# Optimization experiments

Measured on AMD Instinct MI355X. Metric: run time of the kernel, lower is better.

## Reference

```python
import jax, jax.numpy as jnp
import numpy as np
from jax import lax

SCALE = 128.0        # x/y/w/h scale = model input size
MIN_SCORE = 0.5      # min_score_thresh
IOU_THRESH = 0.3     # mediapipe min_suppression_threshold
MAX_DET = 64         # fixed detection slots (jit-safe replacement for dynamic list)
NUM_ANCHORS = 896


def _decode(raw_boxes, anchors):
    # raw_boxes [B,A,16], anchors [A,4] = (x_center, y_center, w, h)
    ax, ay, aw, ah = anchors[:, 0], anchors[:, 1], anchors[:, 2], anchors[:, 3]
    xc = raw_boxes[..., 0] / SCALE * aw + ax
    yc = raw_boxes[..., 1] / SCALE * ah + ay
    w = raw_boxes[..., 2] / SCALE * aw
    h = raw_boxes[..., 3] / SCALE * ah
    box = jnp.stack([yc - h / 2, xc - w / 2, yc + h / 2, xc + w / 2], axis=-1)  # [B,A,4] ymin,xmin,ymax,xmax
    kp = raw_boxes[..., 4:16].reshape(*raw_boxes.shape[:-1], 6, 2)  # [B,A,6,2] (x,y)
    kpx = kp[..., 0] / SCALE * aw[:, None] + ax[:, None]
    kpy = kp[..., 1] / SCALE * ah[:, None] + ay[:, None]
    kps = jnp.stack([kpx, kpy], axis=-1).reshape(*raw_boxes.shape[:-1], 12)
    return jnp.concatenate([box, kps], axis=-1)  # [B,A,16]


def _iou(box, boxes):
    # box [4], boxes [A,4]; coords = ymin,xmin,ymax,xmax
    ymin = jnp.maximum(box[0], boxes[:, 0])
    xmin = jnp.maximum(box[1], boxes[:, 1])
    ymax = jnp.minimum(box[2], boxes[:, 2])
    xmax = jnp.minimum(box[3], boxes[:, 3])
    inter = jnp.maximum(ymax - ymin, 0.0) * jnp.maximum(xmax - xmin, 0.0)
    a1 = jnp.maximum(box[2] - box[0], 0.0) * jnp.maximum(box[3] - box[1], 0.0)
    a2 = jnp.maximum(boxes[:, 2] - boxes[:, 0], 0.0) * jnp.maximum(boxes[:, 3] - boxes[:, 1], 0.0)
    return inter / jnp.maximum(a1 + a2 - inter, 1e-6)


def _weighted_nms_single(coords, scores):
    # coords [A,16], scores [A] -> out [MAX_DET,17] sorted by descending score, zero-padded
    rem = jnp.where(scores >= MIN_SCORE, scores, -1.0)

    def step(rem, _):
        idx = jnp.argmax(rem)
        best = rem[idx]
        iou = _iou(coords[idx, :4], coords[:, :4])
        overlap = (iou > IOU_THRESH) & (rem > 0.0)
        wts = jnp.where(overlap, scores, 0.0)            # weight = candidate score
        denom = jnp.maximum(wts.sum(), 1e-6)
        blended = (coords * wts[:, None]).sum(0) / denom  # weighted box + keypoints
        det = jnp.concatenate([blended, best[None]])
        det = jnp.where(best > 0.0, det, jnp.zeros(17, det.dtype))
        rem = jnp.where(overlap, -1.0, rem)
        return rem, det

    _, out = lax.scan(step, rem, None, length=MAX_DET)
    return out


def _project(dets, matrix):
    # dets [B,MAX_DET,17], matrix [B,8] (first two rows of row-major 4x4 affine)
    m = matrix[:, None, :]  # [B,1,8]
    x_idx = jnp.array([1, 3, 4, 6, 8, 10, 12, 14])
    y_idx = jnp.array([0, 2, 5, 7, 9, 11, 13, 15])
    xs = dets[..., x_idx]
    ys = dets[..., y_idx]
    new_x = xs * m[..., 0:1] + ys * m[..., 1:2] + m[..., 3:4]
    new_y = xs * m[..., 4:5] + ys * m[..., 5:6] + m[..., 7:8]
    out = dets.at[..., x_idx].set(new_x)
    out = out.at[..., y_idx].set(new_y)
    # keep padded (invalid) rows zero, like the segmented-tensor original
    valid = dets[..., 16:17] > 0.0
    return jnp.where(valid, out, 0.0)


def _rescale(dets, h, w):
    hf = jnp.float32(h)
    wf = jnp.float32(w)
    scale = jnp.concatenate([
        jnp.array([1.0, 1.0]) * 0 + jnp.stack([hf, wf]),   # ymin*h, xmin*w
        jnp.stack([hf, wf]),                               # ymax*h, xmax*w
        jnp.tile(jnp.stack([wf, hf]), 6),                  # kp x*w, kp y*h
        jnp.ones((1,), jnp.float32),                       # score unchanged
    ])
    return dets * scale


def setup_inputs() -> dict:
    key = jax.random.key(0)
    k1, k2, k3, k4 = jax.random.split(key, 4)
    B = 2048
    return {
        "raw_boxes": jax.random.normal(k1, (B, NUM_ANCHORS, 16), jnp.float32),
        "raw_scores": jax.random.normal(k2, (B, NUM_ANCHORS), jnp.float32),
        "anchors": jax.random.uniform(k3, (NUM_ANCHORS, 4), jnp.float32),
        "transform_matrix": jax.random.normal(k4, (B, 8), jnp.float32),
        "h": 720,
        "w": 1280,
    }


def reference(raw_boxes, raw_scores, anchors, transform_matrix, h, w):
    coords = _decode(raw_boxes, anchors)                       # [B,A,16]
    scores = jax.nn.sigmoid(jnp.clip(raw_scores, -100.0, 100.0))
    dets = jax.vmap(_weighted_nms_single)(coords, scores)      # [B,MAX_DET,17]
    dets = _project(dets, transform_matrix)
    dets = _rescale(dets, h, w)
    return dets
```

## Files before the change

### kernel.cpp

```cpp
#include <hip/hip_runtime.h>
#include <math.h>

#define NANCH 896
#define MAXD 64
#define MAXSLOTS 14

__device__ __forceinline__ float selv17(const float d[17], int c) {
    float v = d[0];
#pragma unroll
    for (int k = 1; k < 17; ++k) v = (c == k) ? d[k] : v;
    return v;
}

__global__ __launch_bounds__(256, 5) void blaze_kernel(
    const float* __restrict__ raw_boxes,
    const float* __restrict__ raw_scores,
    const float* __restrict__ anchors,
    const float* __restrict__ tmat,
    const int* __restrict__ hptr,
    const int* __restrict__ wptr,
    float* __restrict__ out)
{
    __shared__ float4 sbox[NANCH];
    __shared__ float  sscore[NANCH];
    __shared__ int    sidx[NANCH];
    __shared__ int    wcnt[16];
    __shared__ float  sdet[17];

    const int b    = blockIdx.x;
    const int tid  = threadIdx.x;
    const int lane = tid & 63;
    const int wv   = tid >> 6;

    const float* rb = raw_boxes  + (size_t)b * (NANCH * 16);
    const float* rs = raw_scores + (size_t)b * NANCH;
    const float inv = 1.f / 128.f;

    float sval[4];
    bool  act[4];
#pragma unroll
    for (int r = 0; r < 4; ++r) {
        int a = r * 256 + tid;
        float s = -1.f;
        if (a < NANCH) {
            float x = rs[a];
            x = fminf(fmaxf(x, -100.f), 100.f);
            s = 1.f / (1.f + expf(-x));
        }
        sval[r] = s;
        act[r]  = (s >= 0.5f);
    }
    unsigned long long bm[4];
#pragma unroll
    for (int r = 0; r < 4; ++r) {
        bm[r] = __ballot(act[r]);
        if (lane == 0) wcnt[r * 4 + wv] = __popcll(bm[r]);
    }
    __syncthreads();
    int pos[4];
    int base = 0;
#pragma unroll
    for (int r = 0; r < 4; ++r) {
        int off = base;
        for (int w2 = 0; w2 < wv; ++w2) off += wcnt[r * 4 + w2];
        pos[r] = off + (int)__popcll(bm[r] & ((1ull << lane) - 1ull));
        base += wcnt[r * 4 + 0] + wcnt[r * 4 + 1] + wcnt[r * 4 + 2] + wcnt[r * 4 + 3];
    }
    const int count = base;

#pragma unroll
    for (int r = 0; r < 4; ++r) {
        int a = r * 256 + tid;
        if (act[r]) {
            float4 an = *(const float4*)(anchors + a * 4);
            float4 r0 = *(const float4*)(rb + a * 16);
            float xc = r0.x * inv * an.z + an.x;
            float yc = r0.y * inv * an.w + an.y;
            float ww = r0.z * inv * an.z;
            float hh = r0.w * inv * an.w;
            sbox[pos[r]] = make_float4(yc - hh * 0.5f, xc - ww * 0.5f,
                                       yc + hh * 0.5f, xc + ww * 0.5f);
            sscore[pos[r]] = sval[r];
            sidx[pos[r]]   = a;
        }
    }
    __syncthreads();

    if (wv != 0) return;

    float rem[MAXSLOTS];
#pragma unroll
    for (int j = 0; j < MAXSLOTS; ++j) {
        int i = lane + 64 * j;
        rem[j] = (i < count) ? sscore[i] : -1.f;
    }

    const float* M = tmat + (size_t)b * 8;
    const float m0 = M[0], m1 = M[1], m3 = M[3];
    const float m4 = M[4], m5 = M[5], m7 = M[7];
    const float hf = (float)(*hptr);
    const float wf = (float)(*wptr);
    float* ob = out + (size_t)b * (MAXD * 17);

    int iter = 0;
    while (true) {
        float bv = -2.f; int bi = 1 << 30;
#pragma unroll
        for (int j = 0; j < MAXSLOTS; ++j) {
            if (64 * j < count) {
                if (rem[j] > bv) { bv = rem[j]; bi = lane + 64 * j; }
            }
        }
#pragma unroll
        for (int s2 = 32; s2 >= 1; s2 >>= 1) {
            float ov = __shfl_xor(bv, s2, 64);
            int   oi = __shfl_xor(bi, s2, 64);
            if (ov > bv || (ov == bv && oi < bi)) { bv = ov; bi = oi; }
        }

        if (bv <= 0.f) {
            int n = (MAXD - iter) * 17;
            float* op = ob + iter * 17;
            for (int e = lane; e < n; e += 64) op[e] = 0.f;
            break;
        }

        float4 bb = sbox[bi];
        float a1 = fmaxf(bb.z - bb.x, 0.f) * fmaxf(bb.w - bb.y, 0.f);

        float acc[16];
#pragma unroll
        for (int c = 0; c < 16; ++c) acc[c] = 0.f;
        float wsum = 0.f;
        bool anyov = false;

#pragma unroll
        for (int j = 0; j < MAXSLOTS; ++j) {
            if (64 * j < count) {
                int i = lane + 64 * j;
                bool valid = (i < count) && (rem[j] > 0.f);
                if (valid) {
                    float4 c0 = sbox[i];
                    float ai = fmaxf(c0.z - c0.x, 0.f) * fmaxf(c0.w - c0.y, 0.f);
                    float yA = fmaxf(bb.x, c0.x);
                    float xA = fmaxf(bb.y, c0.y);
                    float yB = fminf(bb.z, c0.z);
                    float xB = fminf(bb.w, c0.w);
                    float inter = fmaxf(yB - yA, 0.f) * fmaxf(xB - xA, 0.f);
                    float iou = inter / fmaxf(a1 + ai - inter, 1e-6f);
                    if (iou > 0.3f) {
                        anyov = true;
                        float wj = sscore[i];
                        rem[j] = -1.f;
                        wsum += wj;
                        acc[0] += c0.x * wj; acc[1] += c0.y * wj;
                        acc[2] += c0.z * wj; acc[3] += c0.w * wj;
                        int a = sidx[i];
                        float4 an = *(const float4*)(anchors + a * 4);
                        const float* rp = rb + a * 16;
                        float4 r1 = *(const float4*)(rp + 4);
                        float4 r2 = *(const float4*)(rp + 8);
                        float4 r3 = *(const float4*)(rp + 12);
                        acc[4]  += (r1.x * inv * an.z + an.x) * wj;
                        acc[5]  += (r1.y * inv * an.w + an.y) * wj;
                        acc[6]  += (r1.z * inv * an.z + an.x) * wj;
                        acc[7]  += (r1.w * inv * an.w + an.y) * wj;
                        acc[8]  += (r2.x * inv * an.z + an.x) * wj;
                        acc[9]  += (r2.y * inv * an.w + an.y) * wj;
                        acc[10] += (r2.z * inv * an.z + an.x) * wj;
                        acc[11] += (r2.w * inv * an.w + an.y) * wj;
                        acc[12] += (r3.x * inv * an.z + an.x) * wj;
                        acc[13] += (r3.y * inv * an.w + an.y) * wj;
                        acc[14] += (r3.z * inv * an.z + an.x) * wj;
                        acc[15] += (r3.w * inv * an.w + an.y) * wj;
                    }
                }
            }
        }

        bool stuck = (__ballot(anyov) == 0ull);

        float det[17];
        if (!stuck) {
#pragma unroll
            for (int s2 = 32; s2 >= 1; s2 >>= 1) {
                wsum += __shfl_xor(wsum, s2, 64);
#pragma unroll
                for (int c = 0; c < 16; ++c) acc[c] += __shfl_xor(acc[c], s2, 64);
            }
            float dnm = fmaxf(wsum, 1e-6f);
#pragma unroll
            for (int c = 0; c < 16; ++c) det[c] = acc[c] / dnm;
        } else {
#pragma unroll
            for (int c = 0; c < 16; ++c) det[c] = 0.f;
        }
        det[16] = bv;

        {
            const int xi[8] = { 1, 3, 4, 6, 8, 10, 12, 14 };
            const int yi[8] = { 0, 2, 5, 7, 9, 11, 13, 15 };
#pragma unroll
            for (int k = 0; k < 8; ++k) {
                float x = det[xi[k]], y = det[yi[k]];
                det[xi[k]] = (x * m0 + y * m1 + m3) * wf;
                det[yi[k]] = (x * m4 + y * m5 + m7) * hf;
            }
        }

        if (stuck) {
            if (lane < 17) sdet[lane] = selv17(det, lane);
            int n = (MAXD - iter) * 17;
            float* op = ob + iter * 17;
            for (int e = lane; e < n; e += 64) {
                int c = e % 17;
                op[e] = sdet[c];
            }
            break;
        } else {
            if (lane < 17) ob[iter * 17 + lane] = selv17(det, lane);
            ++iter;
            if (iter == MAXD) break;
        }
    }
}

extern "C" void kernel_launch(void* const* d_in, const int* in_sizes, int n_in,
                              void* d_out, int out_size, void* d_ws, size_t ws_size,
                              hipStream_t stream) {
    (void)n_in; (void)out_size; (void)d_ws; (void)ws_size;
    const float* raw_boxes  = (const float*)d_in[0];
    const float* raw_scores = (const float*)d_in[1];
    const float* anchors    = (const float*)d_in[2];
    const float* tmat       = (const float*)d_in[3];
    const int*   hptr       = (const int*)d_in[4];
    const int*   wptr       = (const int*)d_in[5];
    float* out = (float*)d_out;

    const int B = in_sizes[0] / (NANCH * 16);
    blaze_kernel<<<B, 256, 0, stream>>>(raw_boxes, raw_scores, anchors, tmat,
                                        hptr, wptr, out);
}
```

Measured before the change: 203.1 us.

## Split decode and NMS into two kernels with one wavefront per image

Decode and compaction of candidates now run in a separate kernel that writes boxes, scores and indices to global workspace. The NMS kernel then packs four images per block, one per wavefront, so all wavefronts do useful work instead of three idling after decode. This removes the large per-block shared memory and lets more NMS wavefronts run at once. In exchange it adds a workspace round-trip through global or L2 memory, a second launch, and box reads from global memory inside the serial NMS loop.

After: 237.8 us. 1.17x slower.

```diff
diff --git a/kernel.cpp b/kernel.cpp
--- a/kernel.cpp
+++ b/kernel.cpp
@@ -12,20 +12,16 @@
     return v;
 }
 
-__global__ __launch_bounds__(256, 5) void blaze_kernel(
+__global__ __launch_bounds__(256) void decode_kernel(
     const float* __restrict__ raw_boxes,
     const float* __restrict__ raw_scores,
     const float* __restrict__ anchors,
-    const float* __restrict__ tmat,
-    const int* __restrict__ hptr,
-    const int* __restrict__ wptr,
-    float* __restrict__ out)
+    float4* __restrict__ wsbox,
+    float*  __restrict__ wsscore,
+    int*    __restrict__ wsidx,
+    int*    __restrict__ wscount)
 {
-    __shared__ float4 sbox[NANCH];
-    __shared__ float  sscore[NANCH];
-    __shared__ int    sidx[NANCH];
-    __shared__ int    wcnt[16];
-    __shared__ float  sdet[17];
+    __shared__ int wcnt[16];
 
     const int b    = blockIdx.x;
     const int tid  = threadIdx.x;
@@ -66,7 +62,10 @@
         pos[r] = off + (int)__popcll(bm[r] & ((1ull << lane) - 1ull));
         base += wcnt[r * 4 + 0] + wcnt[r * 4 + 1] + wcnt[r * 4 + 2] + wcnt[r * 4 + 3];
     }
-    const int count = base;
+
+    float4* obx = wsbox   + (size_t)b * NANCH;
+    float*  osc = wsscore + (size_t)b * NANCH;
+    int*    oix = wsidx   + (size_t)b * NANCH;
 
 #pragma unroll
     for (int r = 0; r < 4; ++r) {
@@ -78,21 +77,51 @@
             float yc = r0.y * inv * an.w + an.y;
             float ww = r0.z * inv * an.z;
             float hh = r0.w * inv * an.w;
-            sbox[pos[r]] = make_float4(yc - hh * 0.5f, xc - ww * 0.5f,
-                                       yc + hh * 0.5f, xc + ww * 0.5f);
-            sscore[pos[r]] = sval[r];
-            sidx[pos[r]]   = a;
-        }
-    }
-    __syncthreads();
-
-    if (wv != 0) return;
+            obx[pos[r]] = make_float4(yc - hh * 0.5f, xc - ww * 0.5f,
+                                      yc + hh * 0.5f, xc + ww * 0.5f);
+            osc[pos[r]] = sval[r];
+            oix[pos[r]] = a;
+        }
+    }
+    if (tid == 0) wscount[b] = base;
+}
+
+__global__ __launch_bounds__(256, 4) void nms_kernel(
+    const float* __restrict__ raw_boxes,
+    const float* __restrict__ anchors,
+    const float* __restrict__ tmat,
+    const int* __restrict__ hptr,
+    const int* __restrict__ wptr,
+    const float4* __restrict__ wsbox,
+    const float*  __restrict__ wsscore,
+    const int*    __restrict__ wsidx,
+    const int*    __restrict__ wscount,
+    float* __restrict__ out,
+    int B)
+{
+    __shared__ float sdet[4][17];
+
+    const int lane = threadIdx.x & 63;
+    const int wv   = threadIdx.x >> 6;
+    const int b    = blockIdx.x * 4 + wv;
+    if (b >= B) return;
+
+    const int count = wscount[b];
+    const float4* bx = wsbox   + (size_t)b * NANCH;
+    const float*  scp= wsscore + (size_t)b * NANCH;
+    const int*    ixp= wsidx   + (size_t)b * NANCH;
+    const float*  rb = raw_boxes + (size_t)b * (NANCH * 16);
+    const float inv = 1.f / 128.f;
 
     float rem[MAXSLOTS];
 #pragma unroll
     for (int j = 0; j < MAXSLOTS; ++j) {
-        int i = lane + 64 * j;
-        rem[j] = (i < count) ? sscore[i] : -1.f;
+        float v = -1.f;
+        if (64 * j < count) {
+            int i = lane + 64 * j;
+            if (i < count) v = scp[i];
+        }
+        rem[j] = v;
     }
 
     const float* M = tmat + (size_t)b * 8;
@@ -125,7 +154,7 @@
             break;
         }
 
-        float4 bb = sbox[bi];
+        float4 bb = bx[bi];
         float a1 = fmaxf(bb.z - bb.x, 0.f) * fmaxf(bb.w - bb.y, 0.f);
 
         float acc[16];
@@ -138,9 +167,8 @@
         for (int j = 0; j < MAXSLOTS; ++j) {
             if (64 * j < count) {
                 int i = lane + 64 * j;
-                bool valid = (i < count) && (rem[j] > 0.f);
-                if (valid) {
-                    float4 c0 = sbox[i];
+                if (i < count && rem[j] > 0.f) {
+                    float4 c0 = bx[i];
                     float ai = fmaxf(c0.z - c0.x, 0.f) * fmaxf(c0.w - c0.y, 0.f);
                     float yA = fmaxf(bb.x, c0.x);
                     float xA = fmaxf(bb.y, c0.y);
@@ -150,12 +178,12 @@
                     float iou = inter / fmaxf(a1 + ai - inter, 1e-6f);
                     if (iou > 0.3f) {
                         anyov = true;
-                        float wj = sscore[i];
+                        float wj = rem[j];
                         rem[j] = -1.f;
                         wsum += wj;
                         acc[0] += c0.x * wj; acc[1] += c0.y * wj;
                         acc[2] += c0.z * wj; acc[3] += c0.w * wj;
-                        int a = sidx[i];
+                        int a = ixp[i];
                         float4 an = *(const float4*)(anchors + a * 4);
                         const float* rp = rb + a * 16;
                         float4 r1 = *(const float4*)(rp + 4);
@@ -209,12 +237,12 @@
         }
 
         if (stuck) {
-            if (lane < 17) sdet[lane] = selv17(det, lane);
+            if (lane < 17) sdet[wv][lane] = selv17(det, lane);
             int n = (MAXD - iter) * 17;
             float* op = ob + iter * 17;
             for (int e = lane; e < n; e += 64) {
                 int c = e % 17;
-                op[e] = sdet[c];
+                op[e] = sdet[wv][c];
             }
             break;
         } else {
@@ -228,7 +256,7 @@
 extern "C" void kernel_launch(void* const* d_in, const int* in_sizes, int n_in,
                               void* d_out, int out_size, void* d_ws, size_t ws_size,
                               hipStream_t stream) {
-    (void)n_in; (void)out_size; (void)d_ws; (void)ws_size;
+    (void)n_in; (void)out_size; (void)ws_size;
     const float* raw_boxes  = (const float*)d_in[0];
     const float* raw_scores = (const float*)d_in[1];
     const float* anchors    = (const float*)d_in[2];
@@ -238,6 +266,17 @@
     float* out = (float*)d_out;
 
     const int B = in_sizes[0] / (NANCH * 16);
-    blaze_kernel<<<B, 256, 0, stream>>>(raw_boxes, raw_scores, anchors, tmat,
-                                        hptr, wptr, out);
-}
+
+    char* ws = (char*)d_ws;
+    float4* wsbox   = (float4*)ws;
+    float*  wsscore = (float*)(ws + (size_t)B * NANCH * 16);
+    int*    wsidx   = (int*)  (ws + (size_t)B * NANCH * 20);
+    int*    wscount = (int*)  (ws + (size_t)B * NANCH * 24);
+
+    decode_kernel<<<B, 256, 0, stream>>>(raw_boxes, raw_scores, anchors,
+                                         wsbox, wsscore, wsidx, wscount);
+    nms_kernel<<<(B + 3) / 4, 256, 0, stream>>>(raw_boxes, anchors, tmat,
+                                                hptr, wptr,
+                                                wsbox, wsscore, wsidx, wscount,
+                                                out, B);
+}
```

## Process one batch per wavefront with register-resident boxes instead of LDS compaction

Applied to the files above, without the earlier changes.

Each 64-lane wavefront now handles a whole batch element, so one block covers four batches. Boxes and scores stay in per-lane register arrays instead of being compacted into shared memory. This removes the block-wide compaction, the __syncthreads barriers, and the three idle waves per block during NMS. The selected box is broadcast with shuffles. The cost is that the IoU loop scans all 14 slots without compaction, register pressure rises (launch bounds drop to 2), and more lanes diverge.

Result: slower. 208.4 us (+2.6%).

```diff
diff --git a/kernel.cpp b/kernel.cpp
--- a/kernel.cpp
+++ b/kernel.cpp
@@ -3,7 +3,7 @@
 
 #define NANCH 896
 #define MAXD 64
-#define MAXSLOTS 14
+#define NS 14
 
 __device__ __forceinline__ float selv17(const float d[17], int c) {
     float v = d[0];
@@ -12,87 +12,46 @@
     return v;
 }
 
-__global__ __launch_bounds__(256, 5) void blaze_kernel(
+__global__ __launch_bounds__(256, 2) void blaze_wave_kernel(
     const float* __restrict__ raw_boxes,
     const float* __restrict__ raw_scores,
     const float* __restrict__ anchors,
     const float* __restrict__ tmat,
     const int* __restrict__ hptr,
     const int* __restrict__ wptr,
-    float* __restrict__ out)
+    float* __restrict__ out,
+    int B)
 {
-    __shared__ float4 sbox[NANCH];
-    __shared__ float  sscore[NANCH];
-    __shared__ int    sidx[NANCH];
-    __shared__ int    wcnt[16];
-    __shared__ float  sdet[17];
-
-    const int b    = blockIdx.x;
-    const int tid  = threadIdx.x;
-    const int lane = tid & 63;
-    const int wv   = tid >> 6;
+    const int lane = threadIdx.x & 63;
+    const int wv   = threadIdx.x >> 6;
+    const int b    = blockIdx.x * 4 + wv;
+    if (b >= B) return;
 
     const float* rb = raw_boxes  + (size_t)b * (NANCH * 16);
     const float* rs = raw_scores + (size_t)b * NANCH;
     const float inv = 1.f / 128.f;
 
-    float sval[4];
-    bool  act[4];
-#pragma unroll
-    for (int r = 0; r < 4; ++r) {
-        int a = r * 256 + tid;
-        float s = -1.f;
-        if (a < NANCH) {
-            float x = rs[a];
-            x = fminf(fmaxf(x, -100.f), 100.f);
-            s = 1.f / (1.f + expf(-x));
-        }
-        sval[r] = s;
-        act[r]  = (s >= 0.5f);
-    }
-    unsigned long long bm[4];
-#pragma unroll
-    for (int r = 0; r < 4; ++r) {
-        bm[r] = __ballot(act[r]);
-        if (lane == 0) wcnt[r * 4 + wv] = __popcll(bm[r]);
-    }
-    __syncthreads();
-    int pos[4];
-    int base = 0;
-#pragma unroll
-    for (int r = 0; r < 4; ++r) {
-        int off = base;
-        for (int w2 = 0; w2 < wv; ++w2) off += wcnt[r * 4 + w2];
-        pos[r] = off + (int)__popcll(bm[r] & ((1ull << lane) - 1ull));
-        base += wcnt[r * 4 + 0] + wcnt[r * 4 + 1] + wcnt[r * 4 + 2] + wcnt[r * 4 + 3];
-    }
-    const int count = base;
-
-#pragma unroll
-    for (int r = 0; r < 4; ++r) {
-        int a = r * 256 + tid;
-        if (act[r]) {
+    float rem[NS], b0[NS], b1[NS], b2[NS], b3[NS];
+#pragma unroll
+    for (int j = 0; j < NS; ++j) {
+        const int a = lane + 64 * j;
+        float x = rs[a];
+        x = fminf(fmaxf(x, -100.f), 100.f);
+        float s = 1.f / (1.f + expf(-x));
+        bool act = (s >= 0.5f);
+        rem[j] = act ? s : -1.f;
+        float t0 = 0.f, t1 = 0.f, t2 = 0.f, t3 = 0.f;
+        if (act) {
             float4 an = *(const float4*)(anchors + a * 4);
             float4 r0 = *(const float4*)(rb + a * 16);
             float xc = r0.x * inv * an.z + an.x;
             float yc = r0.y * inv * an.w + an.y;
             float ww = r0.z * inv * an.z;
             float hh = r0.w * inv * an.w;
-            sbox[pos[r]] = make_float4(yc - hh * 0.5f, xc - ww * 0.5f,
-                                       yc + hh * 0.5f, xc + ww * 0.5f);
-            sscore[pos[r]] = sval[r];
-            sidx[pos[r]]   = a;
-        }
-    }
-    __syncthreads();
-
-    if (wv != 0) return;
-
-    float rem[MAXSLOTS];
-#pragma unroll
-    for (int j = 0; j < MAXSLOTS; ++j) {
-        int i = lane + 64 * j;
-        rem[j] = (i < count) ? sscore[i] : -1.f;
+            t0 = yc - hh * 0.5f; t1 = xc - ww * 0.5f;
+            t2 = yc + hh * 0.5f; t3 = xc + ww * 0.5f;
+        }
+        b0[j] = t0; b1[j] = t1; b2[j] = t2; b3[j] = t3;
     }
 
     const float* M = tmat + (size_t)b * 8;
@@ -106,10 +65,8 @@
     while (true) {
         float bv = -2.f; int bi = 1 << 30;
 #pragma unroll
-        for (int j = 0; j < MAXSLOTS; ++j) {
-            if (64 * j < count) {
-                if (rem[j] > bv) { bv = rem[j]; bi = lane + 64 * j; }
-            }
+        for (int j = 0; j < NS; ++j) {
+            if (rem[j] > bv) { bv = rem[j]; bi = lane + 64 * j; }
         }
 #pragma unroll
         for (int s2 = 32; s2 >= 1; s2 >>= 1) {
@@ -125,8 +82,17 @@
             break;
         }
 
-        float4 bb = sbox[bi];
-        float a1 = fmaxf(bb.z - bb.x, 0.f) * fmaxf(bb.w - bb.y, 0.f);
+        const int bl = bi & 63, bj = bi >> 6;
+        float vb0 = b0[0], vb1 = b1[0], vb2 = b2[0], vb3 = b3[0];
+#pragma unroll
+        for (int j = 1; j < NS; ++j) {
+            if (bj == j) { vb0 = b0[j]; vb1 = b1[j]; vb2 = b2[j]; vb3 = b3[j]; }
+        }
+        const float bby0 = __shfl(vb0, bl, 64);
+        const float bbx0 = __shfl(vb1, bl, 64);
+        const float bby1 = __shfl(vb2, bl, 64);
+        const float bbx1 = __shfl(vb3, bl, 64);
+        const float a1 = fmaxf(bby1 - bby0, 0.f) * fmaxf(bbx1 - bbx0, 0.f);
 
         float acc[16];
 #pragma unroll
@@ -135,45 +101,40 @@
         bool anyov = false;
 
 #pragma unroll
-        for (int j = 0; j < MAXSLOTS; ++j) {
-            if (64 * j < count) {
-                int i = lane + 64 * j;
-                bool valid = (i < count) && (rem[j] > 0.f);
-                if (valid) {
-                    float4 c0 = sbox[i];
-                    float ai = fmaxf(c0.z - c0.x, 0.f) * fmaxf(c0.w - c0.y, 0.f);
-                    float yA = fmaxf(bb.x, c0.x);
-                    float xA = fmaxf(bb.y, c0.y);
-                    float yB = fminf(bb.z, c0.z);
-                    float xB = fminf(bb.w, c0.w);
-                    float inter = fmaxf(yB - yA, 0.f) * fmaxf(xB - xA, 0.f);
-                    float iou = inter / fmaxf(a1 + ai - inter, 1e-6f);
-                    if (iou > 0.3f) {
-                        anyov = true;
-                        float wj = sscore[i];
-                        rem[j] = -1.f;
-                        wsum += wj;
-                        acc[0] += c0.x * wj; acc[1] += c0.y * wj;
-                        acc[2] += c0.z * wj; acc[3] += c0.w * wj;
-                        int a = sidx[i];
-                        float4 an = *(const float4*)(anchors + a * 4);
-                        const float* rp = rb + a * 16;
-                        float4 r1 = *(const float4*)(rp + 4);
-                        float4 r2 = *(const float4*)(rp + 8);
-                        float4 r3 = *(const float4*)(rp + 12);
-                        acc[4]  += (r1.x * inv * an.z + an.x) * wj;
-                        acc[5]  += (r1.y * inv * an.w + an.y) * wj;
-                        acc[6]  += (r1.z * inv * an.z + an.x) * wj;
-                        acc[7]  += (r1.w * inv * an.w + an.y) * wj;
-                        acc[8]  += (r2.x * inv * an.z + an.x) * wj;
-                        acc[9]  += (r2.y * inv * an.w + an.y) * wj;
-                        acc[10] += (r2.z * inv * an.z + an.x) * wj;
-                        acc[11] += (r2.w * inv * an.w + an.y) * wj;
-                        acc[12] += (r3.x * inv * an.z + an.x) * wj;
-                        acc[13] += (r3.y * inv * an.w + an.y) * wj;
-                        acc[14] += (r3.z * inv * an.z + an.x) * wj;
-                        acc[15] += (r3.w * inv * an.w + an.y) * wj;
-                    }
+        for (int j = 0; j < NS; ++j) {
+            if (rem[j] > 0.f) {
+                float ai = fmaxf(b2[j] - b0[j], 0.f) * fmaxf(b3[j] - b1[j], 0.f);
+                float yA = fmaxf(bby0, b0[j]);
+                float xA = fmaxf(bbx0, b1[j]);
+                float yB = fminf(bby1, b2[j]);
+                float xB = fminf(bbx1, b3[j]);
+                float inter = fmaxf(yB - yA, 0.f) * fmaxf(xB - xA, 0.f);
+                float iou = inter / fmaxf(a1 + ai - inter, 1e-6f);
+                if (iou > 0.3f) {
+                    anyov = true;
+                    float wj = rem[j];
+                    rem[j] = -1.f;
+                    wsum += wj;
+                    acc[0] += b0[j] * wj; acc[1] += b1[j] * wj;
+                    acc[2] += b2[j] * wj; acc[3] += b3[j] * wj;
+                    const int a = lane + 64 * j;
+                    float4 an = *(const float4*)(anchors + a * 4);
+                    const float* rp = rb + a * 16;
+                    float4 r1 = *(const float4*)(rp + 4);
+                    float4 r2 = *(const float4*)(rp + 8);
+                    float4 r3 = *(const float4*)(rp + 12);
+                    acc[4]  += (r1.x * inv * an.z + an.x) * wj;
+                    acc[5]  += (r1.y * inv * an.w + an.y) * wj;
+                    acc[6]  += (r1.z * inv * an.z + an.x) * wj;
+                    acc[7]  += (r1.w * inv * an.w + an.y) * wj;
+                    acc[8]  += (r2.x * inv * an.z + an.x) * wj;
+                    acc[9]  += (r2.y * inv * an.w + an.y) * wj;
+                    acc[10] += (r2.z * inv * an.z + an.x) * wj;
+                    acc[11] += (r2.w * inv * an.w + an.y) * wj;
+                    acc[12] += (r3.x * inv * an.z + an.x) * wj;
+                    acc[13] += (r3.y * inv * an.w + an.y) * wj;
+                    acc[14] += (r3.z * inv * an.z + an.x) * wj;
+                    acc[15] += (r3.w * inv * an.w + an.y) * wj;
                 }
             }
         }
@@ -209,13 +170,9 @@
         }
 
         if (stuck) {
-            if (lane < 17) sdet[lane] = selv17(det, lane);
             int n = (MAXD - iter) * 17;
             float* op = ob + iter * 17;
-            for (int e = lane; e < n; e += 64) {
-                int c = e % 17;
-                op[e] = sdet[c];
-            }
+            for (int e = lane; e < n; e += 64) op[e] = selv17(det, e % 17);
             break;
         } else {
             if (lane < 17) ob[iter * 17 + lane] = selv17(det, lane);
@@ -238,6 +195,6 @@
     float* out = (float*)d_out;
 
     const int B = in_sizes[0] / (NANCH * 16);
-    blaze_kernel<<<B, 256, 0, stream>>>(raw_boxes, raw_scores, anchors, tmat,
-                                        hptr, wptr, out);
+    blaze_wave_kernel<<<(B + 3) / 4, 256, 0, stream>>>(raw_boxes, raw_scores, anchors,
+                                                       tmat, hptr, wptr, out, B);
 }
```
